# Performance work log

Hardware: AMD Instinct MI355X
Metric: run time of the kernel (lower is better)

## Reference

```python
import jax, jax.numpy as jnp
import numpy as np

N = 100000
E = 1600000
IN_C = 256
HID = 128
OUT_C = 128
HEADS = 4
C_HEAD = HID // HEADS
BN_EPS = 1e-5
NEG_SLOPE = 0.2


def setup_inputs() -> dict:
    key = jax.random.key(0)
    ks = jax.random.split(key, 12)
    s = lambda fan: 1.0 / np.sqrt(fan)
    return {
        "x": jax.random.normal(ks[0], (N, IN_C), dtype=jnp.float32),
        "W_gat": jax.random.normal(ks[1], (IN_C, HID), dtype=jnp.float32) * s(IN_C),
        "att_src": jax.random.normal(ks[2], (HEADS, C_HEAD), dtype=jnp.float32) * s(C_HEAD),
        "att_dst": jax.random.normal(ks[3], (HEADS, C_HEAD), dtype=jnp.float32) * s(C_HEAD),
        "bias_gat": jnp.zeros((HID,), dtype=jnp.float32),
        "bn1_gamma": jnp.ones((HID,), dtype=jnp.float32),
        "bn1_beta": jnp.zeros((HID,), dtype=jnp.float32),
        "eps_gin": jnp.zeros((), dtype=jnp.float32),
        "lin_W": jax.random.normal(ks[4], (HID, OUT_C), dtype=jnp.float32) * s(HID),
        "lin_b": jnp.zeros((OUT_C,), dtype=jnp.float32),
        "bn2_gamma": jnp.ones((OUT_C,), dtype=jnp.float32),
        "bn2_beta": jnp.zeros((OUT_C,), dtype=jnp.float32),
        "edge_index": jax.random.randint(ks[5], (2, E), 0, N, dtype=jnp.int64),
    }


def batch_norm(h, gamma, beta):
    mu = jnp.mean(h, axis=0)
    var = jnp.var(h, axis=0)
    return (h - mu) * jax.lax.rsqrt(var + BN_EPS) * gamma + beta


def reference(x, W_gat, att_src, att_dst, bias_gat, bn1_gamma, bn1_beta,
              eps_gin, lin_W, lin_b, bn2_gamma, bn2_beta, edge_index):
    src, dst = edge_index[0], edge_index[1]
    # ---- GATConv ----
    h = (x @ W_gat).reshape(N, HEADS, C_HEAD)              # [N,H,C]
    a_src = jnp.einsum('nhc,hc->nh', h, att_src)            # [N,H]
    a_dst = jnp.einsum('nhc,hc->nh', h, att_dst)            # [N,H]
    e = jax.nn.leaky_relu(a_src[src] + a_dst[dst], NEG_SLOPE)  # [E,H]
    # segment softmax over incoming edges of each dst node
    m = jax.ops.segment_max(e, dst, num_segments=N)         # [N,H]
    num = jnp.exp(e - m[dst])                                # [E,H]
    den = jax.ops.segment_sum(num, dst, num_segments=N)      # [N,H]
    alpha = num / den[dst]                                   # [E,H]
    msg = alpha[:, :, None] * h[src]                         # [E,H,C]
    out1 = jax.ops.segment_sum(msg, dst, num_segments=N)     # [N,H,C]
    out1 = out1.reshape(N, HID) + bias_gat
    # BN + ELU (dropout = identity in eval)
    out1 = jax.nn.elu(batch_norm(out1, bn1_gamma, bn1_beta))
    # ---- GINConv: nn((1+eps)*x + sum_neighbors) ----
    agg = jax.ops.segment_sum(out1[src], dst, num_segments=N)
    z = (1.0 + eps_gin) * out1 + agg
    out2 = z @ lin_W + lin_b
    out2 = jax.nn.elu(batch_norm(out2, bn2_gamma, bn2_beta))
    return out2
```

## Files before the change

### kernel.cpp

```cpp
#include <hip/hip_runtime.h>

#define N_NODES 100000
#define N_EDGES 1600000
#define IN_C 256
#define HID 128
#define NEG_SLOPE 0.2f
#define BN_EPS 1e-5f
#define NBUCK 391
#define NPART 391
#define PART_E 4096
#define BPAD 5120
#define TBLOCKS 192
#define NSPLIT 32
#define ELEM_BLOCKS 2048

typedef unsigned int uint32;
typedef __attribute__((ext_vector_type(8))) short bf16x8;
typedef __attribute__((ext_vector_type(4))) float f32x4;

__device__ __forceinline__ float lrelu(float x) { return x > 0.f ? x : NEG_SLOPE * x; }

__device__ __forceinline__ unsigned short f2bf(float f) {
    uint32 u = __float_as_uint(f);
    u += 0x7fffu + ((u >> 16) & 1u);
    return (unsigned short)(u >> 16);
}
__device__ __forceinline__ float bf2f(unsigned short h) {
    return __uint_as_float(((uint32)h) << 16);
}
__device__ __forceinline__ float bflo(uint32 v) { return __uint_as_float(v << 16); }
__device__ __forceinline__ float bfhi(uint32 v) { return __uint_as_float(v & 0xffff0000u); }
__device__ __forceinline__ uint32 packbf(float a, float b) {
    return (uint32)f2bf(a) | ((uint32)f2bf(b) << 16);
}

template <bool AF32, bool OUTF32, bool ATT, bool STATS>
__device__ __forceinline__ void gemm_dev(int bid, const void* __restrict__ Av,
                                         const unsigned short* __restrict__ Wt,
                                         void* __restrict__ Out, int K,
                                         const float* __restrict__ att_s,
                                         const float* __restrict__ att_d,
                                         float* __restrict__ a_src,
                                         float* __restrict__ a_dst,
                                         float* __restrict__ bnst) {
    __shared__ unsigned short As[128 * 72];
    __shared__ unsigned short Bs[128 * 72];
    const int t = threadIdx.x;
    const int n0 = bid * 128;
    const int wv = t >> 6, lane = t & 63;
    const int wy = wv >> 1, wx = wv & 1;
    const int lm = lane & 15, lg = lane >> 4;
    const float* Af = (const float*)Av;
    const unsigned short* Ah = (const unsigned short*)Av;

    f32x4 acc[4][4];
#pragma unroll
    for (int i = 0; i < 4; ++i)
#pragma unroll
        for (int j = 0; j < 4; ++j) acc[i][j] = (f32x4){0.f, 0.f, 0.f, 0.f};

    float4 afp[8];
    uint4 ahp[4];
    uint4 bvp[4];

    if (AF32) {
#pragma unroll
        for (int p = 0; p < 8; ++p) {
            int idx = p * 256 + t, row = idx >> 4, c4 = idx & 15, gn = n0 + row;
            afp[p] = (gn < N_NODES) ? *(const float4*)&Af[(size_t)gn * K + c4 * 4]
                                    : make_float4(0.f, 0.f, 0.f, 0.f);
        }
    } else {
#pragma unroll
        for (int p = 0; p < 4; ++p) {
            int idx = p * 256 + t, row = idx >> 3, c = idx & 7, gn = n0 + row;
            ahp[p] = (gn < N_NODES) ? *(const uint4*)&Ah[(size_t)gn * K + c * 8]
                                    : make_uint4(0, 0, 0, 0);
        }
    }
#pragma unroll
    for (int p = 0; p < 4; ++p) {
        int idx = p * 256 + t, n = idx >> 3, c = idx & 7;
        bvp[p] = *(const uint4*)&Wt[(size_t)n * K + c * 8];
    }

    for (int kc = 0; kc < K; kc += 64) {
        if (AF32) {
#pragma unroll
            for (int p = 0; p < 8; ++p) {
                int idx = p * 256 + t, row = idx >> 4, c4 = idx & 15;
                ushort4 b;
                b.x = f2bf(afp[p].x); b.y = f2bf(afp[p].y);
                b.z = f2bf(afp[p].z); b.w = f2bf(afp[p].w);
                *(ushort4*)&As[row * 72 + c4 * 4] = b;
            }
        } else {
#pragma unroll
            for (int p = 0; p < 4; ++p) {
                int idx = p * 256 + t, row = idx >> 3, c = idx & 7;
                *(uint4*)&As[row * 72 + c * 8] = ahp[p];
            }
        }
#pragma unroll
        for (int p = 0; p < 4; ++p) {
            int idx = p * 256 + t, n = idx >> 3, c = idx & 7;
            *(uint4*)&Bs[n * 72 + c * 8] = bvp[p];
        }
        __syncthreads();
        int kn = kc + 64;
        if (kn < K) {
            if (AF32) {
#pragma unroll
                for (int p = 0; p < 8; ++p) {
                    int idx = p * 256 + t, row = idx >> 4, c4 = idx & 15, gn = n0 + row;
                    afp[p] = (gn < N_NODES) ? *(const float4*)&Af[(size_t)gn * K + kn + c4 * 4]
                                            : make_float4(0.f, 0.f, 0.f, 0.f);
                }
            } else {
#pragma unroll
                for (int p = 0; p < 4; ++p) {
                    int idx = p * 256 + t, row = idx >> 3, c = idx & 7, gn = n0 + row;
                    ahp[p] = (gn < N_NODES) ? *(const uint4*)&Ah[(size_t)gn * K + kn + c * 8]
                                            : make_uint4(0, 0, 0, 0);
                }
            }
#pragma unroll
            for (int p = 0; p < 4; ++p) {
                int idx = p * 256 + t, n = idx >> 3, c = idx & 7;
                bvp[p] = *(const uint4*)&Wt[(size_t)n * K + kn + c * 8];
            }
        }
#pragma unroll
        for (int ks = 0; ks < 2; ++ks) {
            bf16x8 af[4], bfr[4];
#pragma unroll
            for (int i = 0; i < 4; ++i)
                af[i] = *(const bf16x8*)&As[(wy * 64 + i * 16 + lm) * 72 + ks * 32 + lg * 8];
#pragma unroll
            for (int j = 0; j < 4; ++j)
                bfr[j] = *(const bf16x8*)&Bs[(wx * 64 + j * 16 + lm) * 72 + ks * 32 + lg * 8];
#pragma unroll
            for (int i = 0; i < 4; ++i)
#pragma unroll
                for (int j = 0; j < 4; ++j)
                    acc[i][j] = __builtin_amdgcn_mfma_f32_16x16x32_bf16(af[i], bfr[j],
                                                                        acc[i][j], 0, 0, 0);
        }
        __syncthreads();
    }

    float as_w[4], ad_w[4];
    if (ATT) {
#pragma unroll
        for (int j = 0; j < 4; ++j) {
            int col = wx * 64 + j * 16 + lm;
            as_w[j] = att_s[col];
            ad_w[j] = att_d[col];
        }
    }
    float ls[4] = {0.f, 0.f, 0.f, 0.f}, lq[4] = {0.f, 0.f, 0.f, 0.f};
#pragma unroll
    for (int i = 0; i < 4; ++i) {
#pragma unroll
        for (int r = 0; r < 4; ++r) {
            int row = n0 + wy * 64 + i * 16 + lg * 4 + r;
            float v0 = acc[i][0][r], v1 = acc[i][1][r];
            float v2 = acc[i][2][r], v3 = acc[i][3][r];
            if (row < N_NODES) {
                if (OUTF32) {
                    float* op = (float*)Out + (size_t)row * 128 + wx * 64 + lm;
                    op[0] = v0; op[16] = v1; op[32] = v2; op[48] = v3;
                } else {
                    unsigned short* op =
                        (unsigned short*)Out + (size_t)row * 128 + wx * 64 + lm;
                    op[0] = f2bf(v0); op[16] = f2bf(v1);
                    op[32] = f2bf(v2); op[48] = f2bf(v3);
                }
            }
            if (STATS) {
                ls[0] += v0; lq[0] += v0 * v0;
                ls[1] += v1; lq[1] += v1 * v1;
                ls[2] += v2; lq[2] += v2 * v2;
                ls[3] += v3; lq[3] += v3 * v3;
            }
            if (ATT) {
                float ps0 = v0 * as_w[0] + v1 * as_w[1];
                float ps1 = v2 * as_w[2] + v3 * as_w[3];
                float pd0 = v0 * ad_w[0] + v1 * ad_w[1];
                float pd1 = v2 * ad_w[2] + v3 * ad_w[3];
#pragma unroll
                for (int m = 1; m < 16; m <<= 1) {
                    ps0 += __shfl_xor(ps0, m); ps1 += __shfl_xor(ps1, m);
                    pd0 += __shfl_xor(pd0, m); pd1 += __shfl_xor(pd1, m);
                }
                if (lm == 0 && row < N_NODES) {
                    *(float2*)&a_src[row * 4 + wx * 2] = make_float2(ps0, ps1);
                    *(float2*)&a_dst[row * 4 + wx * 2] = make_float2(pd0, pd1);
                }
            }
        }
    }
    if (STATS) {
#pragma unroll
        for (int j = 0; j < 4; ++j) {
            float s = ls[j], q = lq[j];
            s += __shfl_xor(s, 16); s += __shfl_xor(s, 32);
            q += __shfl_xor(q, 16); q += __shfl_xor(q, 32);
            if (lg == 0) {
                int col = wx * 64 + j * 16 + lm;
                atomicAdd(&bnst[col], s);
                atomicAdd(&bnst[128 + col], q);
            }
        }
    }
}

__device__ __forceinline__ void bucket_sort_dev(int b, const int* __restrict__ staging,
                                                const int* __restrict__ cnts,
                                                int* __restrict__ row_ptr,
                                                int* __restrict__ sorted_src) {
    __shared__ int hist[256];
    __shared__ int sh[256];
    __shared__ int spill[256][2];
    __shared__ int spill_cnt;
    __shared__ int obs[4];
    int t = threadIdx.x;
    int part = 0;
    for (int i = t; i < b; i += 256) part += cnts[i];
#pragma unroll
    for (int m = 1; m < 64; m <<= 1) part += __shfl_xor(part, m);
    if ((t & 63) == 0) obs[t >> 6] = part;
    int cnt = cnts[b];
    hist[t] = 0;
    if (t == 0) spill_cnt = 0;
    __syncthreads();
    int ob = obs[0] + obs[1] + obs[2] + obs[3];
    const int* sb = staging + b * BPAD;
    int ent[18], rnk[18];
#pragma unroll
    for (int u = 0; u < 18; ++u) {
        int i = u * 256 + t;
        ent[u] = -1;
        rnk[u] = 0;
        if (i < cnt) {
            int p = sb[i];
            ent[u] = p;
            rnk[u] = atomicAdd(&hist[p >> 17], 1);
        }
    }
    for (int i = 18 * 256 + t; i < cnt; i += 256) {
        int p = sb[i];
        int r = atomicAdd(&hist[p >> 17], 1);
        int si = atomicAdd(&spill_cnt, 1);
        spill[si][0] = p;
        spill[si][1] = r;
    }
    __syncthreads();
    int v0 = hist[t];
    int val = v0;
    sh[t] = val;
    __syncthreads();
    for (int off = 1; off < 256; off <<= 1) {
        int o = (t >= off) ? sh[t - off] : 0;
        __syncthreads();
        val += o;
        sh[t] = val;
        __syncthreads();
    }
    int excl = val - v0;
    int d = b * 256 + t;
    if (d < N_NODES) row_ptr[d] = ob + excl;
    __syncthreads();
    hist[t] = excl;
    __syncthreads();
#pragma unroll
    for (int u = 0; u < 18; ++u) {
        if (ent[u] >= 0) {
            int p = ent[u];
            sorted_src[ob + hist[p >> 17] + rnk[u]] = p & 0x1FFFF;
        }
    }
    for (int i = t; i < spill_cnt; i += 256) {
        int p = spill[i][0];
        sorted_src[ob + hist[p >> 17] + spill[i][1]] = p & 0x1FFFF;
    }
}

__global__ __launch_bounds__(256) void k_prep(const int* __restrict__ ei,
                                              int* __restrict__ gcursor,
                                              int* __restrict__ staging,
                                              const float* __restrict__ W1,
                                              const float* __restrict__ W2,
                                              unsigned short* __restrict__ Wt1,
                                              unsigned short* __restrict__ Wt2,
                                              float* __restrict__ bnstat,
                                              int* __restrict__ row_ptr) {
    int t = threadIdx.x;
    if (blockIdx.x >= NPART) {
        int tb = blockIdx.x - NPART;
        int zi = tb * 256 + t;
        if (zi < NSPLIT * 256 + 256) bnstat[zi] = 0.f;
        if (zi == 0) row_ptr[N_NODES] = N_EDGES;
        int idx = tb * 256 + t;
        if (idx < IN_C * 128) {
            int k = idx >> 7, n = idx & 127;
            Wt1[n * IN_C + k] = f2bf(W1[idx]);
        } else {
            idx -= IN_C * 128;
            if (idx < HID * 128) {
                int k = idx >> 7, n = idx & 127;
                Wt2[n * HID + k] = f2bf(W2[idx]);
            }
        }
        return;
    }
    __shared__ int hist[NBUCK];
    __shared__ int loff[NBUCK];
    __shared__ int gbase[NBUCK];
    __shared__ int lstage[PART_E];
    __shared__ int gaddr[PART_E];
    __shared__ int scanbuf[512];
    int e0 = blockIdx.x * PART_E;
    int cntAll = min(PART_E, N_EDGES - e0);
    for (int i = t; i < NBUCK; i += 256) hist[i] = 0;
    __syncthreads();
    int pk[16];
    short bb[16], rr[16];
#pragma unroll
    for (int u = 0; u < 16; ++u) {
        int e = e0 + u * 256 + t;
        bb[u] = -1;
        rr[u] = 0;
        if (e < N_EDGES) {
            int s = ei[e], d = ei[N_EDGES + e];
            int b = d >> 8;
            int r = atomicAdd(&hist[b], 1);
            pk[u] = ((d & 255) << 17) | s;
            bb[u] = (short)b;
            rr[u] = (short)r;
        }
    }
    __syncthreads();
    scanbuf[t] = (t < NBUCK) ? hist[t] : 0;
    scanbuf[t + 256] = (t + 256 < NBUCK) ? hist[t + 256] : 0;
    __syncthreads();
    for (int off = 1; off < 512; off <<= 1) {
        int a0 = scanbuf[t];
        int a1 = scanbuf[t + 256];
        int b0 = (t >= off) ? scanbuf[t - off] : 0;
        int b1 = (t + 256 >= off) ? scanbuf[t + 256 - off] : 0;
        __syncthreads();
        scanbuf[t] = a0 + b0;
        scanbuf[t + 256] = a1 + b1;
        __syncthreads();
    }
    for (int i = t; i < NBUCK; i += 256) {
        loff[i] = scanbuf[i] - hist[i];
        gbase[i] = hist[i] ? atomicAdd(&gcursor[i], hist[i]) : 0;
    }
    __syncthreads();
#pragma unroll
    for (int u = 0; u < 16; ++u) {
        if (bb[u] >= 0) {
            int b = bb[u], r = rr[u];
            int pos = loff[b] + r;
            lstage[pos] = pk[u];
            gaddr[pos] = b * BPAD + gbase[b] + r;
        }
    }
    __syncthreads();
    for (int i = t; i < cntAll; i += 256) staging[gaddr[i]] = lstage[i];
}

__global__ __launch_bounds__(256) void k_gemm1_sort(const int* __restrict__ staging,
                                                    const int* __restrict__ cnts,
                                                    int* __restrict__ row_ptr,
                                                    int* __restrict__ sorted_src,
                                                    const float* __restrict__ x,
                                                    const unsigned short* __restrict__ Wt1,
                                                    unsigned short* __restrict__ hb,
                                                    const float* __restrict__ att_s,
                                                    const float* __restrict__ att_d,
                                                    float* __restrict__ a_src,
                                                    float* __restrict__ a_dst) {
    if (blockIdx.x < NBUCK) {
        bucket_sort_dev(blockIdx.x, staging, cnts, row_ptr, sorted_src);
    } else {
        gemm_dev<true, false, true, false>(blockIdx.x - NBUCK, x, Wt1, hb, IN_C,
                                           att_s, att_d, a_src, a_dst, nullptr);
    }
}

__global__ __launch_bounds__(256) void k_gemm2(const void* __restrict__ Av,
                                               const unsigned short* __restrict__ Wt,
                                               void* __restrict__ Out,
                                               float* __restrict__ bnst) {
    gemm_dev<false, false, false, true>(blockIdx.x, Av, Wt, Out, HID,
                                        nullptr, nullptr, nullptr, nullptr, bnst);
}

__global__ __launch_bounds__(256) void k_gat_agg(const uint32* __restrict__ h32,
                                                 const float* __restrict__ a_src,
                                                 const float* __restrict__ a_dst,
                                                 const int* __restrict__ row_ptr,
                                                 const int* __restrict__ sorted_src,
                                                 uint32* __restrict__ out1,
                                                 float* __restrict__ bn1p) {
    __shared__ alignas(16) float wbuf[4][4][72];
    __shared__ float sred[4][64][4];
    int lane = threadIdx.x & 63, wv = threadIdx.x >> 6;
    int hd = lane >> 4;
    int node = blockIdx.x * 4 + wv;
    int start = row_ptr[node];
    int deg = row_ptr[node + 1] - start;
    float o0 = 0.f, o1 = 0.f;
    if (deg != 0) {
        float4 ad = *(const float4*)&a_dst[node * 4];
        float acc0 = 0.f, acc1 = 0.f, den = 0.f;
        for (int j0 = 0; j0 < deg; j0 += 64) {
            int m = min(64, deg - j0);
            int s = 0;
            float4 w = make_float4(0.f, 0.f, 0.f, 0.f);
            if (lane < m) {
                s = sorted_src[start + j0 + lane];
                float4 as = *(const float4*)&a_src[s * 4];
                w.x = __expf(lrelu(as.x + ad.x));
                w.y = __expf(lrelu(as.y + ad.y));
                w.z = __expf(lrelu(as.z + ad.z));
                w.w = __expf(lrelu(as.w + ad.w));
            }
            wbuf[wv][0][lane] = w.x;
            wbuf[wv][1][lane] = w.y;
            wbuf[wv][2][lane] = w.z;
            wbuf[wv][3][lane] = w.w;
            __builtin_amdgcn_wave_barrier();
            int e0 = 0;
            for (; e0 + 8 <= m; e0 += 8) {
                uint32 hr[8];
#pragma unroll
                for (int k = 0; k < 8; ++k) {
                    int ss = __builtin_amdgcn_readlane(s, e0 + k);
                    hr[k] = h32[((uint32)ss << 6) + lane];
                }
                float4 w0 = *(const float4*)&wbuf[wv][hd][e0];
                float4 w1 = *(const float4*)&wbuf[wv][hd][e0 + 4];
                float wk[8] = {w0.x, w0.y, w0.z, w0.w, w1.x, w1.y, w1.z, w1.w};
#pragma unroll
                for (int k = 0; k < 8; ++k) {
                    den += wk[k];
                    acc0 = fmaf(wk[k], bflo(hr[k]), acc0);
                    acc1 = fmaf(wk[k], bfhi(hr[k]), acc1);
                }
            }
            for (; e0 < m; ++e0) {
                int ss = __builtin_amdgcn_readlane(s, e0);
                uint32 hv = h32[((uint32)ss << 6) + lane];
                float wk = wbuf[wv][hd][e0];
                den += wk;
                acc0 = fmaf(wk, bflo(hv), acc0);
                acc1 = fmaf(wk, bfhi(hv), acc1);
            }
            __builtin_amdgcn_wave_barrier();
        }
        float rden = 1.f / den;
        o0 = acc0 * rden;
        o1 = acc1 * rden;
    }
    out1[((uint32)node << 6) + lane] = packbf(o0, o1);
    sred[wv][lane][0] = o0;
    sred[wv][lane][1] = o1;
    sred[wv][lane][2] = o0 * o0;
    sred[wv][lane][3] = o1 * o1;
    __syncthreads();
    if (wv == 0) {
        float s0 = sred[0][lane][0] + sred[1][lane][0] + sred[2][lane][0] + sred[3][lane][0];
        float s1 = sred[0][lane][1] + sred[1][lane][1] + sred[2][lane][1] + sred[3][lane][1];
        float q0 = sred[0][lane][2] + sred[1][lane][2] + sred[2][lane][2] + sred[3][lane][2];
        float q1 = sred[0][lane][3] + sred[1][lane][3] + sred[2][lane][3] + sred[3][lane][3];
        float* dst = bn1p + (blockIdx.x & (NSPLIT - 1)) * 256;
        int c0 = lane * 2;
        atomicAdd(&dst[c0], s0);
        atomicAdd(&dst[c0 + 1], s1);
        atomicAdd(&dst[128 + c0], q0);
        atomicAdd(&dst[128 + c0 + 1], q1);
    }
}

__global__ __launch_bounds__(256) void k_gin_agg(const uint32* __restrict__ ob,
                                                 const int* __restrict__ row_ptr,
                                                 const int* __restrict__ sorted_src,
                                                 const float* __restrict__ eps_ptr,
                                                 const float* __restrict__ bn1p,
                                                 const float* __restrict__ gamma,
                                                 const float* __restrict__ beta,
                                                 uint32* __restrict__ zb) {
    __shared__ float stot[256];
    int t = threadIdx.x;
    float v = 0.f;
#pragma unroll
    for (int k = 0; k < NSPLIT; ++k) v += bn1p[k * 256 + t];
    stot[t] = v;
    __syncthreads();
    int lane = t & 63, wv = t >> 6;
    int c0 = lane * 2;
    float mu0 = stot[c0] * (1.f / N_NODES), mu1 = stot[c0 + 1] * (1.f / N_NODES);
    float va0 = stot[128 + c0] * (1.f / N_NODES) - mu0 * mu0;
    float va1 = stot[128 + c0 + 1] * (1.f / N_NODES) - mu1 * mu1;
    float s0 = rsqrtf(va0 + BN_EPS) * gamma[c0];
    float s1 = rsqrtf(va1 + BN_EPS) * gamma[c0 + 1];
    float h0 = beta[c0] - mu0 * s0;
    float h1 = beta[c0 + 1] - mu1 * s1;
    int node = blockIdx.x * 4 + wv;
    int start = row_ptr[node];
    int deg = row_ptr[node + 1] - start;
    float acc0 = 0.f, acc1 = 0.f;
    for (int j0 = 0; j0 < deg; j0 += 64) {
        int m = min(64, deg - j0);
        int s = 0;
        if (lane < m) s = sorted_src[start + j0 + lane];
        int e0 = 0;
        for (; e0 + 8 <= m; e0 += 8) {
            uint32 hr[8];
#pragma unroll
            for (int k = 0; k < 8; ++k) {
                int ss = __builtin_amdgcn_readlane(s, e0 + k);
                hr[k] = ob[((uint32)ss << 6) + lane];
            }
#pragma unroll
            for (int k = 0; k < 8; ++k) {
                float f0 = fmaf(bflo(hr[k]), s0, h0);
                float f1 = fmaf(bfhi(hr[k]), s1, h1);
                acc0 += f0 > 0.f ? f0 : __expf(f0) - 1.f;
                acc1 += f1 > 0.f ? f1 : __expf(f1) - 1.f;
            }
        }
        for (; e0 < m; ++e0) {
            int ss = __builtin_amdgcn_readlane(s, e0);
            uint32 hv = ob[((uint32)ss << 6) + lane];
            float f0 = fmaf(bflo(hv), s0, h0);
            float f1 = fmaf(bfhi(hv), s1, h1);
            acc0 += f0 > 0.f ? f0 : __expf(f0) - 1.f;
            acc1 += f1 > 0.f ? f1 : __expf(f1) - 1.f;
        }
    }
    float ep = 1.f + eps_ptr[0];
    uint32 own = ob[((uint32)node << 6) + lane];
    float f0 = fmaf(bflo(own), s0, h0);
    float f1 = fmaf(bfhi(own), s1, h1);
    f0 = f0 > 0.f ? f0 : __expf(f0) - 1.f;
    f1 = f1 > 0.f ? f1 : __expf(f1) - 1.f;
    zb[((uint32)node << 6) + lane] = packbf(fmaf(ep, f0, acc0), fmaf(ep, f1, acc1));
}

__global__ __launch_bounds__(256) void k_bn_elu_out(const uint32* __restrict__ in,
                                                    const float* __restrict__ acc,
                                                    const float* __restrict__ gamma,
                                                    const float* __restrict__ beta,
                                                    float2* __restrict__ out) {
    int t = threadIdx.x;
    int c0 = (t & 63) * 2;
    float mu0 = acc[c0] * (1.f / N_NODES), mu1 = acc[c0 + 1] * (1.f / N_NODES);
    float va0 = acc[128 + c0] * (1.f / N_NODES) - mu0 * mu0;
    float va1 = acc[128 + c0 + 1] * (1.f / N_NODES) - mu1 * mu1;
    float s0 = rsqrtf(va0 + BN_EPS) * gamma[c0];
    float s1 = rsqrtf(va1 + BN_EPS) * gamma[c0 + 1];
    float h0 = beta[c0] - mu0 * s0;
    float h1 = beta[c0 + 1] - mu1 * s1;
    for (size_t i = (size_t)blockIdx.x * 256 + t; i < (size_t)N_NODES * 64;
         i += (size_t)ELEM_BLOCKS * 256) {
        uint32 v = in[i];
        float r0 = fmaf(bflo(v), s0, h0);
        float r1 = fmaf(bfhi(v), s1, h1);
        r0 = r0 > 0.f ? r0 : __expf(r0) - 1.f;
        r1 = r1 > 0.f ? r1 : __expf(r1) - 1.f;
        out[i] = make_float2(r0, r1);
    }
}

extern "C" void kernel_launch(void* const* d_in, const int* in_sizes, int n_in,
                              void* d_out, int out_size, void* d_ws, size_t ws_size,
                              hipStream_t stream) {
    (void)in_sizes; (void)n_in; (void)out_size; (void)ws_size;
    const float* x       = (const float*)d_in[0];
    const float* W_gat   = (const float*)d_in[1];
    const float* att_src = (const float*)d_in[2];
    const float* att_dst = (const float*)d_in[3];
    const float* bn1_g   = (const float*)d_in[5];
    const float* bn1_b   = (const float*)d_in[6];
    const float* eps_gin = (const float*)d_in[7];
    const float* lin_W   = (const float*)d_in[8];
    const float* bn2_g   = (const float*)d_in[10];
    const float* bn2_b   = (const float*)d_in[11];
    const int*   ei      = (const int*)d_in[12];
    float* out = (float*)d_out;

    char* w = (char*)d_ws;
    size_t o = 0;
    auto take = [&](size_t b) -> char* {
        char* p = w + o;
        o += (b + 255) & ~(size_t)255;
        return p;
    };
    unsigned short* hb   = (unsigned short*)take((size_t)N_NODES * 128 * 2);
    unsigned short* Wt1  = (unsigned short*)take((size_t)128 * IN_C * 2);
    unsigned short* Wt2  = (unsigned short*)take((size_t)128 * HID * 2);
    uint32* o1b          = (uint32*)take((size_t)N_NODES * 64 * 4);
    float* a_src         = (float*)take((size_t)N_NODES * 4 * 4);
    float* a_dst         = (float*)take((size_t)N_NODES * 4 * 4);
    int*   sorted        = (int*)take((size_t)N_EDGES * 4);
    int*   staging       = (int*)take((size_t)NBUCK * BPAD * 4);
    int*   row_ptr       = (int*)take((size_t)(N_NODES + 1) * 4);
    int*   gcursor       = (int*)take((NBUCK + 1) * 4);
    float* bnstat        = (float*)take((NSPLIT * 256 + 256) * 4);
    float* bn1p          = bnstat;
    float* bn2acc        = bnstat + NSPLIT * 256;
    uint32* zb  = (uint32*)hb;
    uint32* o2b = o1b;
    const int nGemmBlocks = (N_NODES + 127) / 128;

    hipMemsetAsync(gcursor, 0, (NBUCK + 1) * sizeof(int), stream);
    k_prep<<<NPART + TBLOCKS, 256, 0, stream>>>(ei, gcursor, staging, W_gat, lin_W,
                                                Wt1, Wt2, bnstat, row_ptr);
    k_gemm1_sort<<<NBUCK + nGemmBlocks, 256, 0, stream>>>(
        staging, gcursor, row_ptr, sorted, x, Wt1, hb, att_src, att_dst, a_src, a_dst);
    k_gat_agg<<<N_NODES / 4, 256, 0, stream>>>((const uint32*)hb, a_src, a_dst, row_ptr,
                                               sorted, o1b, bn1p);
    k_gin_agg<<<N_NODES / 4, 256, 0, stream>>>(o1b, row_ptr, sorted, eps_gin, bn1p,
                                               bn1_g, bn1_b, zb);
    k_gemm2<<<nGemmBlocks, 256, 0, stream>>>(zb, Wt2, o2b, bn2acc);
    k_bn_elu_out<<<ELEM_BLOCKS, 256, 0, stream>>>(o2b, bn2acc, bn2_g, bn2_b,
                                                  (float2*)out);
}
```

Measured before the change: 479.9 us.

## Fuse GEMM2 with BN+ELU via cooperative grid sync; widen GAT aggregation blocks

Adds a cooperative kernel that runs the second GEMM, accumulates the BN statistics, does a grid-wide sync, then applies BN and ELU straight from the accumulators and writes the fp32 output. This removes the bf16 intermediate write and reread plus one kernel launch. The separate two-kernel path stays as a fallback when occupancy is too low or the cooperative launch fails. GAT aggregation blocks also grow from 4 to 8 nodes (512 threads), which halves the number of BN-stat atomics. The risks are the grid-sync cost and the per-call occupancy query overhead.

```diff
diff --git a/kernel.cpp b/kernel.cpp
--- a/kernel.cpp
+++ b/kernel.cpp
@@ -1,4 +1,5 @@
 #include <hip/hip_runtime.h>
+#include <hip/hip_cooperative_groups.h>
 
 #define N_NODES 100000
 #define N_EDGES 1600000
@@ -12,6 +13,7 @@
 #define BPAD 5120
 #define TBLOCKS 192
 #define NSPLIT 32
+#define GAT_NPB 8
 #define ELEM_BLOCKS 2048
 
 typedef unsigned int uint32;
@@ -34,7 +36,7 @@
     return (uint32)f2bf(a) | ((uint32)f2bf(b) << 16);
 }
 
-template <bool AF32, bool OUTF32, bool ATT, bool STATS>
+template <bool AF32, bool OUTF32, bool ATT, bool STATS, bool FUSEBN = false>
 __device__ __forceinline__ void gemm_dev(int bid, const void* __restrict__ Av,
                                          const unsigned short* __restrict__ Wt,
                                          void* __restrict__ Out, int K,
@@ -42,7 +44,10 @@
                                          const float* __restrict__ att_d,
                                          float* __restrict__ a_src,
                                          float* __restrict__ a_dst,
-                                         float* __restrict__ bnst) {
+                                         float* __restrict__ bnst,
+                                         const float* __restrict__ gamma = nullptr,
+                                         const float* __restrict__ beta = nullptr,
+                                         float* __restrict__ fout = nullptr) {
     __shared__ unsigned short As[128 * 72];
     __shared__ unsigned short Bs[128 * 72];
     const int t = threadIdx.x;
@@ -166,15 +171,17 @@
             int row = n0 + wy * 64 + i * 16 + lg * 4 + r;
             float v0 = acc[i][0][r], v1 = acc[i][1][r];
             float v2 = acc[i][2][r], v3 = acc[i][3][r];
-            if (row < N_NODES) {
-                if (OUTF32) {
-                    float* op = (float*)Out + (size_t)row * 128 + wx * 64 + lm;
-                    op[0] = v0; op[16] = v1; op[32] = v2; op[48] = v3;
-                } else {
-                    unsigned short* op =
-                        (unsigned short*)Out + (size_t)row * 128 + wx * 64 + lm;
-                    op[0] = f2bf(v0); op[16] = f2bf(v1);
-                    op[32] = f2bf(v2); op[48] = f2bf(v3);
+            if constexpr (!FUSEBN) {
+                if (row < N_NODES) {
+                    if (OUTF32) {
+                        float* op = (float*)Out + (size_t)row * 128 + wx * 64 + lm;
+                        op[0] = v0; op[16] = v1; op[32] = v2; op[48] = v3;
+                    } else {
+                        unsigned short* op =
+                            (unsigned short*)Out + (size_t)row * 128 + wx * 64 + lm;
+                        op[0] = f2bf(v0); op[16] = f2bf(v1);
+                        op[32] = f2bf(v2); op[48] = f2bf(v3);
+                    }
                 }
             }
             if (STATS) {
@@ -210,6 +217,34 @@
                 int col = wx * 64 + j * 16 + lm;
                 atomicAdd(&bnst[col], s);
                 atomicAdd(&bnst[128 + col], q);
+            }
+        }
+    }
+    if constexpr (FUSEBN) {
+        cooperative_groups::this_grid().sync();
+        float sc[4], sh2[4];
+#pragma unroll
+        for (int j = 0; j < 4; ++j) {
+            int col = wx * 64 + j * 16 + lm;
+            float mu = bnst[col] * (1.f / N_NODES);
+            float var = bnst[128 + col] * (1.f / N_NODES) - mu * mu;
+            sc[j] = rsqrtf(var + BN_EPS) * gamma[col];
+            sh2[j] = beta[col] - mu * sc[j];
+        }
+#pragma unroll
+        for (int i = 0; i < 4; ++i) {
+#pragma unroll
+            for (int r = 0; r < 4; ++r) {
+                int row = n0 + wy * 64 + i * 16 + lg * 4 + r;
+                if (row < N_NODES) {
+                    float* op = fout + (size_t)row * 128 + wx * 64 + lm;
+#pragma unroll
+                    for (int j = 0; j < 4; ++j) {
+                        float v = fmaf(acc[i][j][r], sc[j], sh2[j]);
+                        v = v > 0.f ? v : __expf(v) - 1.f;
+                        op[j * 16] = v;
+                    }
+                }
             }
         }
     }
@@ -391,165 +426,23 @@
     }
 }
 
+__global__ __launch_bounds__(256, 4) void k_gemm2_bn(const void* __restrict__ Av,
+                                                     const unsigned short* __restrict__ Wt,
+                                                     float* __restrict__ bnst,
+                                                     const float* __restrict__ gamma,
+                                                     const float* __restrict__ beta,
+                                                     float* __restrict__ fout) {
+    gemm_dev<false, false, false, true, true>(blockIdx.x, Av, Wt, nullptr, HID,
+                                              nullptr, nullptr, nullptr, nullptr,
+                                              bnst, gamma, beta, fout);
+}
+
 __global__ __launch_bounds__(256) void k_gemm2(const void* __restrict__ Av,
                                                const unsigned short* __restrict__ Wt,
                                                void* __restrict__ Out,
                                                float* __restrict__ bnst) {
     gemm_dev<false, false, false, true>(blockIdx.x, Av, Wt, Out, HID,
                                         nullptr, nullptr, nullptr, nullptr, bnst);
-}
-
-__global__ __launch_bounds__(256) void k_gat_agg(const uint32* __restrict__ h32,
-                                                 const float* __restrict__ a_src,
-                                                 const float* __restrict__ a_dst,
-                                                 const int* __restrict__ row_ptr,
-                                                 const int* __restrict__ sorted_src,
-                                                 uint32* __restrict__ out1,
-                                                 float* __restrict__ bn1p) {
-    __shared__ alignas(16) float wbuf[4][4][72];
-    __shared__ float sred[4][64][4];
-    int lane = threadIdx.x & 63, wv = threadIdx.x >> 6;
-    int hd = lane >> 4;
-    int node = blockIdx.x * 4 + wv;
-    int start = row_ptr[node];
-    int deg = row_ptr[node + 1] - start;
-    float o0 = 0.f, o1 = 0.f;
-    if (deg != 0) {
-        float4 ad = *(const float4*)&a_dst[node * 4];
-        float acc0 = 0.f, acc1 = 0.f, den = 0.f;
-        for (int j0 = 0; j0 < deg; j0 += 64) {
-            int m = min(64, deg - j0);
-            int s = 0;
-            float4 w = make_float4(0.f, 0.f, 0.f, 0.f);
-            if (lane < m) {
-                s = sorted_src[start + j0 + lane];
-                float4 as = *(const float4*)&a_src[s * 4];
-                w.x = __expf(lrelu(as.x + ad.x));
-                w.y = __expf(lrelu(as.y + ad.y));
-                w.z = __expf(lrelu(as.z + ad.z));
-                w.w = __expf(lrelu(as.w + ad.w));
-            }
-            wbuf[wv][0][lane] = w.x;
-            wbuf[wv][1][lane] = w.y;
-            wbuf[wv][2][lane] = w.z;
-            wbuf[wv][3][lane] = w.w;
-            __builtin_amdgcn_wave_barrier();
-            int e0 = 0;
-            for (; e0 + 8 <= m; e0 += 8) {
-                uint32 hr[8];
-#pragma unroll
-                for (int k = 0; k < 8; ++k) {
-                    int ss = __builtin_amdgcn_readlane(s, e0 + k);
-                    hr[k] = h32[((uint32)ss << 6) + lane];
-                }
-                float4 w0 = *(const float4*)&wbuf[wv][hd][e0];
-                float4 w1 = *(const float4*)&wbuf[wv][hd][e0 + 4];
-                float wk[8] = {w0.x, w0.y, w0.z, w0.w, w1.x, w1.y, w1.z, w1.w};
-#pragma unroll
-                for (int k = 0; k < 8; ++k) {
-                    den += wk[k];
-                    acc0 = fmaf(wk[k], bflo(hr[k]), acc0);
-                    acc1 = fmaf(wk[k], bfhi(hr[k]), acc1);
-                }
-            }
-            for (; e0 < m; ++e0) {
-                int ss = __builtin_amdgcn_readlane(s, e0);
-                uint32 hv = h32[((uint32)ss << 6) + lane];
-                float wk = wbuf[wv][hd][e0];
-                den += wk;
-                acc0 = fmaf(wk, bflo(hv), acc0);
-                acc1 = fmaf(wk, bfhi(hv), acc1);
-            }
-            __builtin_amdgcn_wave_barrier();
-        }
-        float rden = 1.f / den;
-        o0 = acc0 * rden;
-        o1 = acc1 * rden;
-    }
-    out1[((uint32)node << 6) + lane] = packbf(o0, o1);
-    sred[wv][lane][0] = o0;
-    sred[wv][lane][1] = o1;
-    sred[wv][lane][2] = o0 * o0;
-    sred[wv][lane][3] = o1 * o1;
-    __syncthreads();
-    if (wv == 0) {
-        float s0 = sred[0][lane][0] + sred[1][lane][0] + sred[2][lane][0] + sred[3][lane][0];
-        float s1 = sred[0][lane][1] + sred[1][lane][1] + sred[2][lane][1] + sred[3][lane][1];
-        float q0 = sred[0][lane][2] + sred[1][lane][2] + sred[2][lane][2] + sred[3][lane][2];
-        float q1 = sred[0][lane][3] + sred[1][lane][3] + sred[2][lane][3] + sred[3][lane][3];
-        float* dst = bn1p + (blockIdx.x & (NSPLIT - 1)) * 256;
-        int c0 = lane * 2;
-        atomicAdd(&dst[c0], s0);
-        atomicAdd(&dst[c0 + 1], s1);
-        atomicAdd(&dst[128 + c0], q0);
-        atomicAdd(&dst[128 + c0 + 1], q1);
-    }
-}
-
-__global__ __launch_bounds__(256) void k_gin_agg(const uint32* __restrict__ ob,
-                                                 const int* __restrict__ row_ptr,
-                                                 const int* __restrict__ sorted_src,
-                                                 const float* __restrict__ eps_ptr,
-                                                 const float* __restrict__ bn1p,
-                                                 const float* __restrict__ gamma,
-                                                 const float* __restrict__ beta,
-                                                 uint32* __restrict__ zb) {
-    __shared__ float stot[256];
-    int t = threadIdx.x;
-    float v = 0.f;
-#pragma unroll
-    for (int k = 0; k < NSPLIT; ++k) v += bn1p[k * 256 + t];
-    stot[t] = v;
-    __syncthreads();
-    int lane = t & 63, wv = t >> 6;
-    int c0 = lane * 2;
-    float mu0 = stot[c0] * (1.f / N_NODES), mu1 = stot[c0 + 1] * (1.f / N_NODES);
-    float va0 = stot[128 + c0] * (1.f / N_NODES) - mu0 * mu0;
-    float va1 = stot[128 + c0 + 1] * (1.f / N_NODES) - mu1 * mu1;
-    float s0 = rsqrtf(va0 + BN_EPS) * gamma[c0];
-    float s1 = rsqrtf(va1 + BN_EPS) * gamma[c0 + 1];
-    float h0 = beta[c0] - mu0 * s0;
-    float h1 = beta[c0 + 1] - mu1 * s1;
-    int node = blockIdx.x * 4 + wv;
-    int start = row_ptr[node];
-    int deg = row_ptr[node + 1] - start;
-    float acc0 = 0.f, acc1 = 0.f;
-    for (int j0 = 0; j0 < deg; j0 += 64) {
-        int m = min(64, deg - j0);
-        int s = 0;
-        if (lane < m) s = sorted_src[start + j0 + lane];
-        int e0 = 0;
-        for (; e0 + 8 <= m; e0 += 8) {
-            uint32 hr[8];
-#pragma unroll
-            for (int k = 0; k < 8; ++k) {
-                int ss = __builtin_amdgcn_readlane(s, e0 + k);
-                hr[k] = ob[((uint32)ss << 6) + lane];
-            }
-#pragma unroll
-            for (int k = 0; k < 8; ++k) {
-                float f0 = fmaf(bflo(hr[k]), s0, h0);
-                float f1 = fmaf(bfhi(hr[k]), s1, h1);
-                acc0 += f0 > 0.f ? f0 : __expf(f0) - 1.f;
-                acc1 += f1 > 0.f ? f1 : __expf(f1) - 1.f;
-            }
-        }
-        for (; e0 < m; ++e0) {
-            int ss = __builtin_amdgcn_readlane(s, e0);
-            uint32 hv = ob[((uint32)ss << 6) + lane];
-            float f0 = fmaf(bflo(hv), s0, h0);
-            float f1 = fmaf(bfhi(hv), s1, h1);
-            acc0 += f0 > 0.f ? f0 : __expf(f0) - 1.f;
-            acc1 += f1 > 0.f ? f1 : __expf(f1) - 1.f;
-        }
-    }
-    float ep = 1.f + eps_ptr[0];
-    uint32 own = ob[((uint32)node << 6) + lane];
-    float f0 = fmaf(bflo(own), s0, h0);
-    float f1 = fmaf(bfhi(own), s1, h1);
-    f0 = f0 > 0.f ? f0 : __expf(f0) - 1.f;
-    f1 = f1 > 0.f ? f1 : __expf(f1) - 1.f;
-    zb[((uint32)node << 6) + lane] = packbf(fmaf(ep, f0, acc0), fmaf(ep, f1, acc1));
 }
 
 __global__ __launch_bounds__(256) void k_bn_elu_out(const uint32* __restrict__ in,
@@ -575,6 +468,161 @@
         r1 = r1 > 0.f ? r1 : __expf(r1) - 1.f;
         out[i] = make_float2(r0, r1);
     }
+}
+
+__global__ __launch_bounds__(512) void k_gat_agg(const uint32* __restrict__ h32,
+                                                 const float* __restrict__ a_src,
+                                                 const float* __restrict__ a_dst,
+                                                 const int* __restrict__ row_ptr,
+                                                 const int* __restrict__ sorted_src,
+                                                 uint32* __restrict__ out1,
+                                                 float* __restrict__ bn1p) {
+    __shared__ alignas(16) float wbuf[GAT_NPB][4][72];
+    __shared__ float sred[GAT_NPB][64][4];
+    int lane = threadIdx.x & 63, wv = threadIdx.x >> 6;
+    int hd = lane >> 4;
+    int node = blockIdx.x * GAT_NPB + wv;
+    int start = row_ptr[node];
+    int deg = row_ptr[node + 1] - start;
+    float o0 = 0.f, o1 = 0.f;
+    if (deg != 0) {
+        float4 ad = *(const float4*)&a_dst[node * 4];
+        float acc0 = 0.f, acc1 = 0.f, den = 0.f;
+        for (int j0 = 0; j0 < deg; j0 += 64) {
+            int m = min(64, deg - j0);
+            int s = 0;
+            float4 w = make_float4(0.f, 0.f, 0.f, 0.f);
+            if (lane < m) {
+                s = sorted_src[start + j0 + lane];
+                float4 as = *(const float4*)&a_src[s * 4];
+                w.x = __expf(lrelu(as.x + ad.x));
+                w.y = __expf(lrelu(as.y + ad.y));
+                w.z = __expf(lrelu(as.z + ad.z));
+                w.w = __expf(lrelu(as.w + ad.w));
+            }
+            wbuf[wv][0][lane] = w.x;
+            wbuf[wv][1][lane] = w.y;
+            wbuf[wv][2][lane] = w.z;
+            wbuf[wv][3][lane] = w.w;
+            __builtin_amdgcn_wave_barrier();
+            int e0 = 0;
+            for (; e0 + 8 <= m; e0 += 8) {
+                uint32 hr[8];
+#pragma unroll
+                for (int k = 0; k < 8; ++k) {
+                    int ss = __builtin_amdgcn_readlane(s, e0 + k);
+                    hr[k] = h32[((uint32)ss << 6) + lane];
+                }
+                float4 w0 = *(const float4*)&wbuf[wv][hd][e0];
+                float4 w1 = *(const float4*)&wbuf[wv][hd][e0 + 4];
+                float wk[8] = {w0.x, w0.y, w0.z, w0.w, w1.x, w1.y, w1.z, w1.w};
+#pragma unroll
+                for (int k = 0; k < 8; ++k) {
+                    den += wk[k];
+                    acc0 = fmaf(wk[k], bflo(hr[k]), acc0);
+                    acc1 = fmaf(wk[k], bfhi(hr[k]), acc1);
+                }
+            }
+            for (; e0 < m; ++e0) {
+                int ss = __builtin_amdgcn_readlane(s, e0);
+                uint32 hv = h32[((uint32)ss << 6) + lane];
+                float wk = wbuf[wv][hd][e0];
+                den += wk;
+                acc0 = fmaf(wk, bflo(hv), acc0);
+                acc1 = fmaf(wk, bfhi(hv), acc1);
+            }
+            __builtin_amdgcn_wave_barrier();
+        }
+        float rden = 1.f / den;
+        o0 = acc0 * rden;
+        o1 = acc1 * rden;
+    }
+    out1[((uint32)node << 6) + lane] = packbf(o0, o1);
+    sred[wv][lane][0] = o0;
+    sred[wv][lane][1] = o1;
+    sred[wv][lane][2] = o0 * o0;
+    sred[wv][lane][3] = o1 * o1;
+    __syncthreads();
+    if (wv == 0) {
+        float s0 = 0.f, s1 = 0.f, q0 = 0.f, q1 = 0.f;
+#pragma unroll
+        for (int g = 0; g < GAT_NPB; ++g) {
+            s0 += sred[g][lane][0]; s1 += sred[g][lane][1];
+            q0 += sred[g][lane][2]; q1 += sred[g][lane][3];
+        }
+        float* dst = bn1p + (blockIdx.x & (NSPLIT - 1)) * 256;
+        int c0 = lane * 2;
+        atomicAdd(&dst[c0], s0);
+        atomicAdd(&dst[c0 + 1], s1);
+        atomicAdd(&dst[128 + c0], q0);
+        atomicAdd(&dst[128 + c0 + 1], q1);
+    }
+}
+
+__global__ __launch_bounds__(256) void k_gin_agg(const uint32* __restrict__ ob,
+                                                 const int* __restrict__ row_ptr,
+                                                 const int* __restrict__ sorted_src,
+                                                 const float* __restrict__ eps_ptr,
+                                                 const float* __restrict__ bn1p,
+                                                 const float* __restrict__ gamma,
+                                                 const float* __restrict__ beta,
+                                                 uint32* __restrict__ zb) {
+    __shared__ float stot[256];
+    int t = threadIdx.x;
+    float v = 0.f;
+#pragma unroll
+    for (int k = 0; k < NSPLIT; ++k) v += bn1p[k * 256 + t];
+    stot[t] = v;
+    __syncthreads();
+    int lane = t & 63, wv = t >> 6;
+    int c0 = lane * 2;
+    float mu0 = stot[c0] * (1.f / N_NODES), mu1 = stot[c0 + 1] * (1.f / N_NODES);
+    float va0 = stot[128 + c0] * (1.f / N_NODES) - mu0 * mu0;
+    float va1 = stot[128 + c0 + 1] * (1.f / N_NODES) - mu1 * mu1;
+    float s0 = rsqrtf(va0 + BN_EPS) * gamma[c0];
+    float s1 = rsqrtf(va1 + BN_EPS) * gamma[c0 + 1];
+    float h0 = beta[c0] - mu0 * s0;
+    float h1 = beta[c0 + 1] - mu1 * s1;
+    int node = blockIdx.x * 4 + wv;
+    int start = row_ptr[node];
+    int deg = row_ptr[node + 1] - start;
+    float acc0 = 0.f, acc1 = 0.f;
+    for (int j0 = 0; j0 < deg; j0 += 64) {
+        int m = min(64, deg - j0);
+        int s = 0;
+        if (lane < m) s = sorted_src[start + j0 + lane];
+        int e0 = 0;
+        for (; e0 + 8 <= m; e0 += 8) {
+            uint32 hr[8];
+#pragma unroll
+            for (int k = 0; k < 8; ++k) {
+                int ss = __builtin_amdgcn_readlane(s, e0 + k);
+                hr[k] = ob[((uint32)ss << 6) + lane];
+            }
+#pragma unroll
+            for (int k = 0; k < 8; ++k) {
+                float f0 = fmaf(bflo(hr[k]), s0, h0);
+                float f1 = fmaf(bfhi(hr[k]), s1, h1);
+                acc0 += f0 > 0.f ? f0 : __expf(f0) - 1.f;
+                acc1 += f1 > 0.f ? f1 : __expf(f1) - 1.f;
+            }
+        }
+        for (; e0 < m; ++e0) {
+            int ss = __builtin_amdgcn_readlane(s, e0);
+            uint32 hv = ob[((uint32)ss << 6) + lane];
+            float f0 = fmaf(bflo(hv), s0, h0);
+            float f1 = fmaf(bfhi(hv), s1, h1);
+            acc0 += f0 > 0.f ? f0 : __expf(f0) - 1.f;
+            acc1 += f1 > 0.f ? f1 : __expf(f1) - 1.f;
+        }
+    }
+    float ep = 1.f + eps_ptr[0];
+    uint32 own = ob[((uint32)node << 6) + lane];
+    float f0 = fmaf(bflo(own), s0, h0);
+    float f1 = fmaf(bfhi(own), s1, h1);
+    f0 = f0 > 0.f ? f0 : __expf(f0) - 1.f;
+    f1 = f1 > 0.f ? f1 : __expf(f1) - 1.f;
+    zb[((uint32)node << 6) + lane] = packbf(fmaf(ep, f0, acc0), fmaf(ep, f1, acc1));
 }
 
 extern "C" void kernel_launch(void* const* d_in, const int* in_sizes, int n_in,
@@ -623,11 +671,30 @@
                                                 Wt1, Wt2, bnstat, row_ptr);
     k_gemm1_sort<<<NBUCK + nGemmBlocks, 256, 0, stream>>>(
         staging, gcursor, row_ptr, sorted, x, Wt1, hb, att_src, att_dst, a_src, a_dst);
-    k_gat_agg<<<N_NODES / 4, 256, 0, stream>>>((const uint32*)hb, a_src, a_dst, row_ptr,
-                                               sorted, o1b, bn1p);
+    k_gat_agg<<<N_NODES / GAT_NPB, 512, 0, stream>>>((const uint32*)hb, a_src, a_dst,
+                                                     row_ptr, sorted, o1b, bn1p);
     k_gin_agg<<<N_NODES / 4, 256, 0, stream>>>(o1b, row_ptr, sorted, eps_gin, bn1p,
                                                bn1_g, bn1_b, zb);
-    k_gemm2<<<nGemmBlocks, 256, 0, stream>>>(zb, Wt2, o2b, bn2acc);
-    k_bn_elu_out<<<ELEM_BLOCKS, 256, 0, stream>>>(o2b, bn2acc, bn2_g, bn2_b,
-                                                  (float2*)out);
-}
+
+    bool coop = false;
+    int maxb = 0;
+    if (hipOccupancyMaxActiveBlocksPerMultiprocessor(&maxb, k_gemm2_bn, 256, 0) ==
+            hipSuccess &&
+        maxb * 256 >= nGemmBlocks) {
+        const void* zav = (const void*)zb;
+        const unsigned short* wt2v = Wt2;
+        float* bnv = bn2acc;
+        const float* gv = bn2_g;
+        const float* bv = bn2_b;
+        float* fov = out;
+        void* kargs[] = {&zav, &wt2v, &bnv, &gv, &bv, &fov};
+        if (hipLaunchCooperativeKernel(k_gemm2_bn, dim3(nGemmBlocks), dim3(256),
+                                       kargs, 0, stream) == hipSuccess)
+            coop = true;
+    }
+    if (!coop) {
+        k_gemm2<<<nGemmBlocks, 256, 0, stream>>>(zb, Wt2, o2b, bn2acc);
+        k_bn_elu_out<<<ELEM_BLOCKS, 256, 0, stream>>>(o2b, bn2acc, bn2_g, bn2_b,
+                                                      (float2*)out);
+    }
+}
```

Measured after the change: 466.2 us. -2.9%, faster.
